# Kernel optimization log

Measured on AMD Instinct MI355X. Metric: run time of the kernel, lower is better.

The kernel has to match this reference:

```python
import jax, jax.numpy as jnp
import numpy as np

E, H, VS, VT, B, S, T = 256, 512, 32000, 32000, 64, 40, 40

def setup_inputs() -> dict:
    key = jax.random.key(0)
    ks = jax.random.split(key, 32)
    def n(k, shape, scale=0.05):
        return (jax.random.normal(k, shape, jnp.float32) * scale)
    return {
        "source_padded": jax.random.randint(ks[0], (B, S), 0, VS),
        "target_padded": jax.random.randint(ks[1], (B, T), 0, VT),
        "source_lengths": jax.random.randint(ks[2], (B,), 2, S + 1),
        "src_emb": n(ks[3], (VS, E)), "tgt_emb": n(ks[4], (VT, E)),
        "Wih_f": n(ks[5], (4 * H, E)), "Whh_f": n(ks[6], (4 * H, H)), "b_f": jnp.zeros((4 * H,), jnp.float32),
        "Wih_b": n(ks[7], (4 * H, E)), "Whh_b": n(ks[8], (4 * H, H)), "b_b": jnp.zeros((4 * H,), jnp.float32),
        "Wih_d": n(ks[9], (4 * H, H + E)), "Whh_d": n(ks[10], (4 * H, H)), "b_d": jnp.zeros((4 * H,), jnp.float32),
        "Whp": n(ks[11], (H, 2 * H)), "bhp": jnp.zeros((H,), jnp.float32),
        "Wcp": n(ks[12], (H, 2 * H)), "bcp": jnp.zeros((H,), jnp.float32),
        "Watt": n(ks[13], (H, 2 * H)), "batt": jnp.zeros((H,), jnp.float32),
        "Wcomb": n(ks[14], (H, 3 * H)), "bcomb": jnp.zeros((H,), jnp.float32),
        "Wvoc": n(ks[15], (VT, H)), "bvoc": jnp.zeros((VT,), jnp.float32),
    }

def _lstm_cell(x, h, c, Wih, Whh, b):
    g = x @ Wih.T + h @ Whh.T + b
    i, f, gg, o = jnp.split(g, 4, axis=-1)  # PyTorch gate order i,f,g,o
    c = jax.nn.sigmoid(f) * c + jax.nn.sigmoid(i) * jnp.tanh(gg)
    h = jax.nn.sigmoid(o) * jnp.tanh(c)
    return h, c

def _masked_scan(X, lengths, Wih, Whh, b):
    # X: [B,S,E]; emulates packed LSTM: state frozen and output zeroed past length
    Bn, Sn, _ = X.shape
    Hn = Whh.shape[1]
    def step(carry, inp):
        h, c = carry
        xt, t = inp
        hn, cn = _lstm_cell(xt, h, c, Wih, Whh, b)
        valid = (t < lengths)[:, None]
        h = jnp.where(valid, hn, h)
        c = jnp.where(valid, cn, c)
        return (h, c), jnp.where(valid, h, 0.0)
    init = (jnp.zeros((Bn, Hn), X.dtype), jnp.zeros((Bn, Hn), X.dtype))
    (h, c), outs = jax.lax.scan(step, init, (X.transpose(1, 0, 2), jnp.arange(Sn)))
    return outs.transpose(1, 0, 2), h, c

def _rev_in_len(X, lengths):
    # reverse each sequence within its own length, zeros elsewhere
    Sn = X.shape[1]
    idx = lengths[:, None] - 1 - jnp.arange(Sn)[None, :]
    g = jnp.take_along_axis(X, jnp.clip(idx, 0)[..., None], axis=1)
    return jnp.where((idx >= 0)[..., None], g, 0.0)

def _forward(source_padded, target_padded, source_lengths,
             src_emb, tgt_emb, Wih_f, Whh_f, b_f, Wih_b, Whh_b, b_b,
             Wih_d, Whh_d, b_d, Whp, bhp, Wcp, bcp, Watt, batt,
             Wcomb, bcomb, Wvoc, bvoc):
    X = src_emb[source_padded]                              # [B,S,E]
    out_f, hf, cf = _masked_scan(X, source_lengths, Wih_f, Whh_f, b_f)
    Xr = _rev_in_len(X, source_lengths)
    out_r, hb, cb = _masked_scan(Xr, source_lengths, Wih_b, Whh_b, b_b)
    out_b = _rev_in_len(out_r, source_lengths)
    enc_hidden = jnp.concatenate([out_f, out_b], axis=-1)   # [B,S,2H]
    dec_h = jnp.concatenate([hf, hb], axis=-1) @ Whp.T + bhp
    dec_c = jnp.concatenate([cf, cb], axis=-1) @ Wcp.T + bcp

    # generate_sent_masks: 1 at positions 1..len-1 (faithful to source), then masked_fill(-inf) where 1
    pos = jnp.arange(S)[None, :]
    enc_masks = (pos >= 1) & (pos < source_lengths[:, None])  # [B,S] bool

    enc_proj = enc_hidden @ Watt.T + batt                    # [B,S,H]
    Y = tgt_emb[target_padded]                               # [B,T,E]
    Hn = Whh_d.shape[1]
    o0 = jnp.zeros((B, Hn), jnp.float32)

    def dec_step(carry, y_t):
        h, c, o_prev = carry
        ybar = jnp.concatenate([y_t, o_prev], axis=-1)
        h, c = _lstm_cell(ybar, h, c, Wih_d, Whh_d, b_d)
        e = jnp.einsum('bsh,bh->bs', enc_proj, h)
        e = jnp.where(enc_masks, -jnp.inf, e)
        alpha = jax.nn.softmax(e, axis=-1)
        a = jnp.einsum('bs,bsd->bd', alpha, enc_hidden)      # [B,2H]
        U = jnp.concatenate([h, a], axis=-1)                 # [B,3H]
        O = jnp.tanh(U @ Wcomb.T + bcomb)                    # dropout eval-mode identity
        return (h, c, O), O

    _, outs = jax.lax.scan(dec_step, (dec_h, dec_c, o0), Y.transpose(1, 0, 2))  # [T,B,H]
    logits = outs @ Wvoc.T + bvoc                            # [T,B,VT]
    logp = jax.nn.log_softmax(logits, axis=-1)
    # CrossEntropyLoss(P.permute(1,2,0), target): mean NLL over all B*T positions
    tgt = target_padded.T[..., None]                         # [T,B,1]
    nll = -jnp.take_along_axis(logp, tgt, axis=-1).squeeze(-1)
    return nll.mean()

def reference(source_padded, target_padded, source_lengths,
              src_emb, tgt_emb, Wih_f, Whh_f, b_f, Wih_b, Whh_b, b_b,
              Wih_d, Whh_d, b_d, Whp, bhp, Wcp, bcp, Watt, batt,
              Wcomb, bcomb, Wvoc, bvoc):
    return _forward(source_padded, target_padded, source_lengths,
                    src_emb, tgt_emb, Wih_f, Whh_f, b_f, Wih_b, Whh_b, b_b,
                    Wih_d, Whh_d, b_d, Whp, bhp, Wcp, bcp, Watt, batt,
                    Wcomb, bcomb, Wvoc, bvoc)
```

## Files before the change

kernel.cpp:

```cpp
#include <hip/hip_runtime.h>
#include <math.h>

#define En 256
#define Hn 512
#define Bn 64
#define Sn 40
#define Tn 40
#define VTn 32000
#define Rn (Tn*Bn)
#define NCH 500

typedef short v8s __attribute__((ext_vector_type(8)));
typedef float v4f __attribute__((ext_vector_type(4)));
typedef _Float16 h2v __attribute__((ext_vector_type(2)));

#if defined(__has_builtin)
#  if __has_builtin(__builtin_amdgcn_fdot2)
#    define HAVE_FDOT2 1
#  endif
#endif

__device__ __forceinline__ float dot4(float4 a, float4 b){
  return a.x*b.x + a.y*b.y + a.z*b.z + a.w*b.w;
}
__device__ __forceinline__ float sigm(float x){ return 1.f/(1.f+__expf(-x)); }
__device__ __forceinline__ unsigned short f2bf(float f){
  unsigned u = __float_as_uint(f);
  unsigned r = u + 0x7FFFu + ((u>>16)&1u);
  return (unsigned short)(r>>16);
}
__device__ __forceinline__ float bf2f(unsigned short u){
  return __uint_as_float(((unsigned)u)<<16);
}
__device__ __forceinline__ unsigned pkbf(float a, float b){
  return (unsigned)f2bf(a) | ((unsigned)f2bf(b)<<16);
}
__device__ __forceinline__ unsigned pkh(float a, float b){
  _Float16 ha = (_Float16)a, hb = (_Float16)b;
  unsigned short ua = __builtin_bit_cast(unsigned short, ha);
  unsigned short ub = __builtin_bit_cast(unsigned short, hb);
  return (unsigned)ua | ((unsigned)ub<<16);
}
__device__ __forceinline__ float fd2(unsigned w, unsigned h, float c){
#ifdef HAVE_FDOT2
  return __builtin_amdgcn_fdot2(__builtin_bit_cast(h2v,w), __builtin_bit_cast(h2v,h), c, false);
#else
  h2v a = __builtin_bit_cast(h2v,w), b = __builtin_bit_cast(h2v,h);
  return c + (float)a[0]*(float)b[0] + (float)a[1]*(float)b[1];
#endif
}

__global__ void prep(float* zero_base,
                     const int* __restrict__ src, const int* __restrict__ tgt,
                     const int* __restrict__ lens, int* __restrict__ grev,
                     int* __restrict__ gtgt,
                     const float* __restrict__ Whh_f, unsigned short* __restrict__ Whf16,
                     const float* __restrict__ Whh_b, unsigned short* __restrict__ Whb16,
                     const float* __restrict__ Whh_d, const float* __restrict__ Wih_d,
                     unsigned short* __restrict__ Wd16,
                     const float* __restrict__ Wcomb, unsigned short* __restrict__ Wc16){
  int blk = blockIdx.x, tid = threadIdx.x;
  if (blk < 209){
    ((float4*)zero_base)[blk*256 + tid] = make_float4(0.f,0.f,0.f,0.f);
    return;
  }
  blk -= 209;
  if (blk < 10){
    int r = blk*256 + tid;
    if (r < Bn*Sn){
      int b = r/Sn, s = r%Sn;
      int j = lens[b]-1-s;
      grev[r] = (j>=0) ? src[b*Sn+j] : -1;
      int t2 = r>>6, b2 = r&63;
      gtgt[r] = tgt[b2*Tn + t2];
    }
    return;
  }
  blk -= 10;
  if (blk < 512){
    size_t e = ((size_t)blk*256 + tid)*8;
    float4 a = *(const float4*)(Whh_f+e), b = *(const float4*)(Whh_f+e+4);
    uint4 u; u.x=pkbf(a.x,a.y); u.y=pkbf(a.z,a.w); u.z=pkbf(b.x,b.y); u.w=pkbf(b.z,b.w);
    *(uint4*)(Whf16+e) = u;
    return;
  }
  blk -= 512;
  if (blk < 512){
    size_t e = ((size_t)blk*256 + tid)*8;
    float4 a = *(const float4*)(Whh_b+e), b = *(const float4*)(Whh_b+e+4);
    uint4 u; u.x=pkbf(a.x,a.y); u.y=pkbf(a.z,a.w); u.z=pkbf(b.x,b.y); u.w=pkbf(b.z,b.w);
    *(uint4*)(Whb16+e) = u;
    return;
  }
  blk -= 512;
  if (blk < 1024){
    size_t e = ((size_t)blk*256 + tid)*8;
    int row = (int)(e>>10), k = (int)(e&1023);
    const float* sp = (k<512) ? (Whh_d + (size_t)row*512 + k)
                              : (Wih_d + (size_t)row*768 + 256 + (k-512));
    float4 a = *(const float4*)sp, b = *(const float4*)(sp+4);
    uint4 u; u.x=pkbf(a.x,a.y); u.y=pkbf(a.z,a.w); u.z=pkbf(b.x,b.y); u.w=pkbf(b.z,b.w);
    *(uint4*)(Wd16+e) = u;
    return;
  }
  blk -= 1024;
  {
    size_t e = ((size_t)blk*256 + tid)*8;
    float4 a = *(const float4*)(Wcomb+e), b = *(const float4*)(Wcomb+e+4);
    uint4 u; u.x=pkh(a.x,a.y); u.y=pkh(a.z,a.w); u.z=pkh(b.x,b.y); u.w=pkh(b.z,b.w);
    *(uint4*)(Wc16+e) = u;
  }
}

struct GArg {
  const float* A; const int* gth; int lda;
  const float* B; int ldb;
  const float* bias; float* C; int ldc; int K;
};
struct GArg3 { GArg a[3]; };

__global__ __launch_bounds__(256) void ggemm(GArg3 p3){
  GArg d = p3.a[blockIdx.z];
  __shared__ unsigned short Abf[128*64];
  __shared__ unsigned short Bbf[128*64];
  const int n0 = blockIdx.x*128, r0 = blockIdx.y*128;
  const int tid = threadIdx.x;
  const int w = tid>>6, lane = tid&63;
  const int wr = w>>1, wc = w&1;
  v4f acc[4][4];
#pragma unroll
  for (int i=0;i<4;++i)
#pragma unroll
    for (int j=0;j<4;++j) acc[i][j] = (v4f){0.f,0.f,0.f,0.f};
  const int srow = tid>>1, kc = (tid&1)*32;
  int ar = d.gth ? d.gth[r0+srow] : (r0+srow);
  const float* Arow = (ar>=0) ? (d.A + (size_t)ar*d.lda) : nullptr;
  const float* Brow = d.B + (size_t)(n0+srow)*d.ldb;
  for (int kb=0; kb<d.K; kb+=64){
    __syncthreads();
#pragma unroll
    for (int c=0;c<4;++c){
      int k = kc + c*8;
      int swz = k ^ ((srow&7)<<3);
      uint4 ua;
      if (Arow){
        float4 x0 = *(const float4*)(Arow+kb+k);
        float4 x1 = *(const float4*)(Arow+kb+k+4);
        ua.x=pkbf(x0.x,x0.y); ua.y=pkbf(x0.z,x0.w); ua.z=pkbf(x1.x,x1.y); ua.w=pkbf(x1.z,x1.w);
      } else ua = make_uint4(0,0,0,0);
      *(uint4*)&Abf[srow*64 + swz] = ua;
      float4 y0 = *(const float4*)(Brow+kb+k);
      float4 y1 = *(const float4*)(Brow+kb+k+4);
      uint4 ub; ub.x=pkbf(y0.x,y0.y); ub.y=pkbf(y0.z,y0.w); ub.z=pkbf(y1.x,y1.y); ub.w=pkbf(y1.z,y1.w);
      *(uint4*)&Bbf[srow*64 + swz] = ub;
    }
    __syncthreads();
#pragma unroll
    for (int kk=0; kk<64; kk+=32){
      int kfr = kk + (lane>>4)*8;
      v8s bfr[4];
#pragma unroll
      for (int ni=0;ni<4;++ni){
        int brow = wc*64 + ni*16 + (lane&15);
        bfr[ni] = *(const v8s*)&Bbf[brow*64 + (kfr ^ ((brow&7)<<3))];
      }
#pragma unroll
      for (int mi=0;mi<4;++mi){
        int arl = wr*64 + mi*16 + (lane&15);
        v8s af = *(const v8s*)&Abf[arl*64 + (kfr ^ ((arl&7)<<3))];
#pragma unroll
        for (int ni=0;ni<4;++ni)
          acc[mi][ni] = __builtin_amdgcn_mfma_f32_16x16x32_bf16(af, bfr[ni], acc[mi][ni], 0,0,0);
      }
    }
  }
#pragma unroll
  for (int ni=0;ni<4;++ni){
    int col = n0 + wc*64 + ni*16 + (lane&15);
    float bb = d.bias[col];
#pragma unroll
    for (int mi=0;mi<4;++mi)
#pragma unroll
      for (int r=0;r<4;++r){
        int row = r0 + wr*64 + mi*16 + (lane>>4)*4 + r;
        d.C[(size_t)row*d.ldc + col] = acc[mi][ni][r] + bb;
      }
  }
}

__global__ __launch_bounds__(256) void enc_step(
    const unsigned short* __restrict__ hf_in, unsigned short* __restrict__ hf_out,
    const unsigned short* __restrict__ hb_in, unsigned short* __restrict__ hb_out,
    float* __restrict__ cF, float* __restrict__ cB,
    const unsigned short* __restrict__ Wf16, const unsigned short* __restrict__ Wb16,
    const float* __restrict__ Gf, const float* __restrict__ Gb,
    float* __restrict__ encH, float* __restrict__ outR,
    const int* __restrict__ lens,
    const float* __restrict__ Wvoc, unsigned short* __restrict__ W16, int s){
  const int bxall = blockIdx.x;
  const int tid = threadIdx.x;
  if (bxall >= 64){
    int chunk = s*200 + (bxall - 64);
    if (chunk < 8000){
      size_t e = ((size_t)chunk*256 + tid)*8;
      float4 a = *(const float4*)(Wvoc+e), b = *(const float4*)(Wvoc+e+4);
      uint4 u; u.x=pkbf(a.x,a.y); u.y=pkbf(a.z,a.w); u.z=pkbf(b.x,b.y); u.w=pkbf(b.z,b.w);
      *(uint4*)(W16+e) = u;
    }
    return;
  }
  __shared__ unsigned short Wls[64*64];
  __shared__ unsigned short Hls[64*64];
  __shared__ float Cls[64][66];
  const int bx = bxall;
  const int dir = bx>>5;
  const int u0 = (bx&31)*16;
  const unsigned short* Wm16 = dir ? Wb16 : Wf16;
  const unsigned short* hin = dir ? hb_in : hf_in;
  unsigned short* hout      = dir ? hb_out : hf_out;
  float* c = dir ? cB : cF;
  const float* G = dir ? Gb : Gf;
  const int w = tid>>6, lane = tid&63;
  v4f acc[4];
#pragma unroll
  for (int ni=0;ni<4;++ni) acc[ni] = (v4f){0.f,0.f,0.f,0.f};
  const int l = tid>>2;
  const int kc4 = (tid&3)*16;
  const int grow = (l>>4)*512 + u0 + (l&15);
  const unsigned short* Wrow = Wm16 + (size_t)grow*512;
  const unsigned short* Hrow = hin + (size_t)l*512;
  for (int kb=0; kb<512; kb+=64){
    __syncthreads();
#pragma unroll
    for (int c2=0;c2<2;++c2){
      int k = kc4 + c2*8;
      int swz = k ^ ((l&7)<<3);
      *(uint4*)&Wls[l*64+swz] = *(const uint4*)(Wrow + kb + k);
      *(uint4*)&Hls[l*64+swz] = *(const uint4*)(Hrow + kb + k);
    }
    __syncthreads();
#pragma unroll
    for (int kk=0; kk<64; kk+=32){
      int kfr = kk + (lane>>4)*8;
      int mrow = w*16 + (lane&15);
      v8s af = *(const v8s*)&Wls[mrow*64 + (kfr ^ ((mrow&7)<<3))];
#pragma unroll
      for (int ni=0;ni<4;++ni){
        int brow = ni*16 + (lane&15);
        v8s bf = *(const v8s*)&Hls[brow*64 + (kfr ^ ((brow&7)<<3))];
        acc[ni] = __builtin_amdgcn_mfma_f32_16x16x32_bf16(af, bf, acc[ni], 0,0,0);
      }
    }
  }
#pragma unroll
  for (int ni=0;ni<4;++ni)
#pragma unroll
    for (int r=0;r<4;++r)
      Cls[w*16 + (lane>>4)*4 + r][ni*16 + (lane&15)] = acc[ni][r];
  __syncthreads();
  const int u_l = tid&15, bq = tid>>4;
#pragma unroll
  for (int j=0;j<4;++j){
    int b = bq + j*16;
    size_t gidx = ((size_t)(b*Sn+s))*2048 + u0 + u_l;
    float gi = Cls[u_l][b]      + G[gidx];
    float gf = Cls[16+u_l][b]   + G[gidx+512];
    float gg = Cls[32+u_l][b]   + G[gidx+1024];
    float go = Cls[48+u_l][b]   + G[gidx+1536];
    int bu = b*512 + u0 + u_l;
    bool valid = s < lens[b];
    float cp = c[bu];
    float cn = sigm(gf)*cp + sigm(gi)*tanhf(gg);
    float hn = sigm(go)*tanhf(cn);
    c[bu] = valid ? cn : cp;
    hout[bu] = valid ? f2bf(hn) : hin[bu];
    if (dir==0) encH[((size_t)(b*Sn+s))*1024 + u0+u_l] = valid ? hn : 0.f;
    else        outR[((size_t)(b*Sn+s))*512  + u0+u_l] = valid ? hn : 0.f;
  }
}

__global__ void mid_fused(const unsigned short* __restrict__ h16f,
                          const unsigned short* __restrict__ h16b,
                          const float* __restrict__ cF, const float* __restrict__ cB,
                          const float* __restrict__ Whp, const float* __restrict__ bhp,
                          const float* __restrict__ Wcp, const float* __restrict__ bcp,
                          unsigned short* __restrict__ ho0, float* __restrict__ dC,
                          const float* __restrict__ outR, const int* __restrict__ lens,
                          float* __restrict__ encH){
  int blk = blockIdx.x, tid = threadIdx.x;
  if (blk < 128){
    int isC = blk >= 64;
    int idx = (blk & 63)*256 + tid;
#pragma unroll
    for (int e=0;e<2;++e){
      int o = idx*2 + e;
      int b = o>>9, u = o&511;
      if (!isC){
        const float* wr = Whp + (size_t)u*1024;
        float acc = bhp[u];
        const uint4* hf4 = (const uint4*)(h16f + (size_t)b*512);
        for (int q=0;q<64;++q){
          uint4 v = hf4[q];
          unsigned uu[4] = {v.x,v.y,v.z,v.w};
#pragma unroll
          for (int i2=0;i2<4;++i2){
            acc += bf2f((unsigned short)(uu[i2]&0xFFFF))*wr[q*8+i2*2];
            acc += bf2f((unsigned short)(uu[i2]>>16))   *wr[q*8+i2*2+1];
          }
        }
        const uint4* hb4 = (const uint4*)(h16b + (size_t)b*512);
        const float* wr2 = wr + 512;
        for (int q=0;q<64;++q){
          uint4 v = hb4[q];
          unsigned uu[4] = {v.x,v.y,v.z,v.w};
#pragma unroll
          for (int i2=0;i2<4;++i2){
            acc += bf2f((unsigned short)(uu[i2]&0xFFFF))*wr2[q*8+i2*2];
            acc += bf2f((unsigned short)(uu[i2]>>16))   *wr2[q*8+i2*2+1];
          }
        }
        ho0[b*1024 + u] = f2bf(acc);
      } else {
        const float4* w4 = (const float4*)(Wcp + (size_t)u*1024);
        float acc = bcp[u];
        const float4* x1 = (const float4*)(cF + (size_t)b*512);
        const float4* x2 = (const float4*)(cB + (size_t)b*512);
        for (int q=0;q<128;++q) acc += dot4(x1[q], w4[q]);
        for (int q=0;q<128;++q) acc += dot4(x2[q], w4[128+q]);
        dC[b*512 + u] = acc;
      }
    }
    return;
  }
  blk -= 128;
  {
    int e = (blk*256 + tid)*8;
    int u = e & 511;
    int bsi = e >> 9;
    int s = bsi % Sn, b = bsi / Sn;
    int len = lens[b];
    float4 v0 = make_float4(0,0,0,0), v1 = make_float4(0,0,0,0);
    if (s < len){
      int j = len-1-s;
      const float* sp = outR + ((size_t)(b*Sn+j))*512 + u;
      v0 = *(const float4*)sp; v1 = *(const float4*)(sp+4);
    }
    float* dp = encH + ((size_t)(b*Sn+s))*1024 + 512 + u;
    *(float4*)dp = v0; *(float4*)(dp+4) = v1;
  }
}

__global__ __launch_bounds__(256) void dec_gates(
    const unsigned short* __restrict__ Wd16, const unsigned short* __restrict__ ho_cur,
    unsigned short* __restrict__ ho_next, const float* __restrict__ Gdy,
    float* __restrict__ dC, int t){
  __shared__ unsigned short Wls[64*64];
  __shared__ unsigned short Hls[64*64];
  __shared__ float Cls[64][66];
  const int u0 = blockIdx.x*16;
  const int tid = threadIdx.x, w = tid>>6, lane = tid&63;
  v4f acc[4];
#pragma unroll
  for (int ni=0;ni<4;++ni) acc[ni] = (v4f){0.f,0.f,0.f,0.f};
  const int l = tid>>2;
  const int kc4 = (tid&3)*16;
  const int grow = (l>>4)*512 + u0 + (l&15);
  const unsigned short* Wrow = Wd16 + (size_t)grow*1024;
  const unsigned short* Hrow = ho_cur + (size_t)l*1024;
  for (int kb=0; kb<1024; kb+=64){
    __syncthreads();
#pragma unroll
    for (int c2=0;c2<2;++c2){
      int k = kc4 + c2*8;
      int swz = k ^ ((l&7)<<3);
      *(uint4*)&Wls[l*64+swz] = *(const uint4*)(Wrow + kb + k);
      *(uint4*)&Hls[l*64+swz] = *(const uint4*)(Hrow + kb + k);
    }
    __syncthreads();
#pragma unroll
    for (int kk=0; kk<64; kk+=32){
      int kfr = kk + (lane>>4)*8;
      int mrow = w*16 + (lane&15);
      v8s af = *(const v8s*)&Wls[mrow*64 + (kfr ^ ((mrow&7)<<3))];
#pragma unroll
      for (int ni=0;ni<4;++ni){
        int brow = ni*16 + (lane&15);
        v8s bf = *(const v8s*)&Hls[brow*64 + (kfr ^ ((brow&7)<<3))];
        acc[ni] = __builtin_amdgcn_mfma_f32_16x16x32_bf16(af, bf, acc[ni], 0,0,0);
      }
    }
  }
#pragma unroll
  for (int ni=0;ni<4;++ni)
#pragma unroll
    for (int r=0;r<4;++r)
      Cls[w*16 + (lane>>4)*4 + r][ni*16 + (lane&15)] = acc[ni][r];
  __syncthreads();
  const int u_l = tid&15, bq = tid>>4;
#pragma unroll
  for (int j=0;j<4;++j){
    int b = bq + j*16;
    size_t gidx = ((size_t)(t*Bn+b))*2048 + u0 + u_l;
    float gi = Cls[u_l][b]      + Gdy[gidx];
    float gf = Cls[16+u_l][b]   + Gdy[gidx+512];
    float gg = Cls[32+u_l][b]   + Gdy[gidx+1024];
    float go = Cls[48+u_l][b]   + Gdy[gidx+1536];
    int bu = b*512 + u0 + u_l;
    float cp = dC[bu];
    float cn = sigm(gf)*cp + sigm(gi)*tanhf(gg);
    float hn = sigm(go)*tanhf(cn);
    dC[bu] = cn;
    ho_next[b*1024 + u0 + u_l] = f2bf(hn);
  }
}

__global__ __launch_bounds__(256) void dec_attcomb(
    unsigned short* __restrict__ ho_next, const float* __restrict__ eprj,
    const float* __restrict__ encH, const int* __restrict__ lens,
    const unsigned short* __restrict__ Wc16, const float* __restrict__ bcomb,
    unsigned short* __restrict__ A16, int t){
  const int b = blockIdx.x >> 2;
  const int q = blockIdx.x & 3;
  const int tid = threadIdx.x;
  __shared__ __align__(16) float hs[512];
  __shared__ __align__(16) float als[1024];
  __shared__ float es[Sn], sal[Sn];
  __shared__ float sinv;
  __shared__ __align__(16) unsigned int ha16[768];
  __shared__ float ps[128][2];
  for (int i=tid; i<512; i+=256) hs[i] = bf2f(ho_next[b*1024 + i]);
  __syncthreads();
  const int wv = tid>>6, lane = tid&63;
  const int len = lens[b];
  for (int si=0; si<10; ++si){
    int s2 = wv*10 + si;
    const float* pr = eprj + ((size_t)(b*Sn+s2))*512 + lane*8;
    float4 p0 = *(const float4*)pr, p1 = *(const float4*)(pr+4);
    const float* hh = hs + lane*8;
    float4 h0 = *(const float4*)hh, h1 = *(const float4*)(hh+4);
    float a = dot4(p0,h0) + dot4(p1,h1);
#pragma unroll
    for (int off=32; off; off>>=1) a += __shfl_down(a, off);
    if (lane==0) es[s2] = (s2>=1 && s2<len) ? -INFINITY : a;
  }
  __syncthreads();
  if (tid < 64){
    float e2 = (tid<Sn) ? es[tid] : -INFINITY;
    float m = e2;
#pragma unroll
    for (int off=32; off; off>>=1) m = fmaxf(m, __shfl_xor(m, off));
    float p = (tid<Sn) ? __expf(e2-m) : 0.f;
    float sum = p;
#pragma unroll
    for (int off=32; off; off>>=1) sum += __shfl_xor(sum, off);
    if (tid<Sn) sal[tid] = p;
    if (tid==0) sinv = 1.f/sum;
  }
  __syncthreads();
  float inv = sinv;
#pragma unroll
  for (int dq=0; dq<4; ++dq){
    int d = dq*256 + tid;
    float acc = 0.f;
    for (int s2=0; s2<Sn; ++s2) acc += sal[s2]*encH[((size_t)(b*Sn+s2))*1024 + d];
    als[d] = acc*inv;
  }
  __syncthreads();
  for (int p=tid; p<768; p+=256){
    int i0 = 2*p, i1 = 2*p+1;
    float x0 = (i0<512) ? hs[i0] : als[i0-512];
    float x1 = (i1<512) ? hs[i1] : als[i1-512];
    ha16[p] = pkh(x0, x1);
  }
  __syncthreads();
  const int rloc = tid & 127;
  const int kh = tid >> 7;
  const int row = q*128 + rloc;
  const uint4* wp = (const uint4*)(Wc16 + (size_t)row*1536 + kh*768);
  const uint4* hp = (const uint4*)&ha16[kh*384];
  float a0 = 0.f;
#pragma unroll 4
  for (int qq=0; qq<96; ++qq){
    uint4 wv4 = wp[qq];
    uint4 hv4 = hp[qq];
    a0 = fd2(wv4.x, hv4.x, a0);
    a0 = fd2(wv4.y, hv4.y, a0);
    a0 = fd2(wv4.z, hv4.z, a0);
    a0 = fd2(wv4.w, hv4.w, a0);
  }
  ps[rloc][kh] = a0;
  __syncthreads();
  if (tid < 128){
    int r2 = q*128 + tid;
    float O = tanhf(ps[tid][0] + ps[tid][1] + bcomb[r2]);
    unsigned short ob = f2bf(O);
    ho_next[b*1024 + 512 + r2] = ob;
    A16[((size_t)(t*Bn+b))*512 + r2] = ob;
  }
}

__global__ __launch_bounds__(256) void vocab_mfma(
    const unsigned short* __restrict__ A16, const unsigned short* __restrict__ W16,
    const float* __restrict__ bv, float* __restrict__ stats){
  __shared__ unsigned short Abf[128*64];
  __shared__ unsigned short Bbf[128*64];
  const int vb = blockIdx.x, rb = blockIdx.y;
  const int r0 = rb*128, v0 = vb*128;
  const int tid = threadIdx.x;
  const int w = tid>>6, lane = tid&63;
  const int wr = w>>1, wc = w&1;
  v4f acc[4][4];
#pragma unroll
  for (int i=0;i<4;++i)
#pragma unroll
    for (int j=0;j<4;++j) acc[i][j] = (v4f){0.f,0.f,0.f,0.f};
  const int srow = tid>>1;
  const int sk0  = (tid&1)*8;
  const int arow = wr*64 + (lane&15);
  const int brow = wc*64 + (lane&15);
  const int kfrag = (lane>>4)*8;
  for (int ks=0; ks<8; ++ks){
    const int kb = ks*64;
    __syncthreads();
#pragma unroll
    for (int c=0;c<4;++c){
      int k = sk0 + c*16;
      int swz = k ^ ((srow&7)<<3);
      *(uint4*)&Abf[srow*64 + swz] = *(const uint4*)(A16 + (size_t)(r0+srow)*512 + kb + k);
      *(uint4*)&Bbf[srow*64 + swz] = *(const uint4*)(W16 + (size_t)(v0+srow)*512 + kb + k);
    }
    __syncthreads();
#pragma unroll
    for (int kk=0; kk<64; kk+=32){
      v8s af[4], bf[4];
#pragma unroll
      for (int mi=0;mi<4;++mi){
        int row = arow + mi*16;
        int k = kk + kfrag;
        af[mi] = *(const v8s*)&Abf[row*64 + (k ^ ((row&7)<<3))];
      }
#pragma unroll
      for (int ni=0;ni<4;++ni){
        int row = brow + ni*16;
        int k = kk + kfrag;
        bf[ni] = *(const v8s*)&Bbf[row*64 + (k ^ ((row&7)<<3))];
      }
#pragma unroll
      for (int mi=0;mi<4;++mi)
#pragma unroll
        for (int ni=0;ni<4;++ni)
          acc[mi][ni] = __builtin_amdgcn_mfma_f32_16x16x32_bf16(af[mi], bf[ni], acc[mi][ni], 0,0,0);
    }
  }
  float bj[4];
#pragma unroll
  for (int ni=0;ni<4;++ni) bj[ni] = bv[v0 + wc*64 + ni*16 + (lane&15)];
#pragma unroll
  for (int mi=0;mi<4;++mi){
#pragma unroll
    for (int r=0;r<4;++r){
      float x0 = acc[mi][0][r]+bj[0], x1 = acc[mi][1][r]+bj[1];
      float x2 = acc[mi][2][r]+bj[2], x3 = acc[mi][3][r]+bj[3];
      float mx = fmaxf(fmaxf(x0,x1), fmaxf(x2,x3));
#pragma unroll
      for (int off=1; off<16; off<<=1) mx = fmaxf(mx, __shfl_xor(mx, off));
      float se = __expf(x0-mx)+__expf(x1-mx)+__expf(x2-mx)+__expf(x3-mx);
#pragma unroll
      for (int off=1; off<16; off<<=1) se += __shfl_xor(se, off);
      if ((lane&15)==0){
        int row = r0 + wr*64 + mi*16 + (lane>>4)*4 + r;
        int chunk = vb*2 + wc;
        size_t o = ((size_t)row*NCH + chunk)*2;
        stats[o]   = mx;
        stats[o+1] = se;
      }
    }
  }
}

__global__ void tail(const float* __restrict__ stats, const unsigned short* __restrict__ A16,
                     const float* __restrict__ Wvoc, const float* __restrict__ bvoc,
                     const int* __restrict__ gtgt, float* __restrict__ out){
  int r = blockIdx.x*4 + (threadIdx.x>>6);
  int lane = threadIdx.x & 63;
  const float* st = stats + (size_t)r*NCH*2;
  float M = -INFINITY;
  for (int c=lane; c<NCH; c+=64) M = fmaxf(M, st[2*c]);
#pragma unroll
  for (int off=32; off; off>>=1) M = fmaxf(M, __shfl_xor(M, off));
  float S = 0.f;
  for (int c=lane; c<NCH; c+=64) S += __expf(st[2*c]-M)*st[2*c+1];
#pragma unroll
  for (int off=32; off; off>>=1) S += __shfl_xor(S, off);
  int v = gtgt[r];
  int k = lane*8;
  uint4 a4 = *(const uint4*)(A16 + (size_t)r*512 + k);
  const float* wvp = Wvoc + (size_t)v*512 + k;
  float4 w0 = *(const float4*)wvp, w1 = *(const float4*)(wvp+4);
  unsigned uu[4] = {a4.x, a4.y, a4.z, a4.w};
  float dot = 0.f;
  dot += bf2f((unsigned short)(uu[0]&0xFFFF))*w0.x + bf2f((unsigned short)(uu[0]>>16))*w0.y;
  dot += bf2f((unsigned short)(uu[1]&0xFFFF))*w0.z + bf2f((unsigned short)(uu[1]>>16))*w0.w;
  dot += bf2f((unsigned short)(uu[2]&0xFFFF))*w1.x + bf2f((unsigned short)(uu[2]>>16))*w1.y;
  dot += bf2f((unsigned short)(uu[3]&0xFFFF))*w1.z + bf2f((unsigned short)(uu[3]>>16))*w1.w;
#pragma unroll
  for (int off=32; off; off>>=1) dot += __shfl_down(dot, off);
  if (lane==0){
    float lse = M + logf(S);
    float nll = lse - (dot + bvoc[v]);
    atomicAdd(out, nll * (1.0f/(float)Rn));
  }
}

extern "C" void kernel_launch(void* const* d_in, const int* in_sizes, int n_in,
                              void* d_out, int out_size, void* d_ws, size_t ws_size,
                              hipStream_t stream){
  (void)in_sizes; (void)n_in; (void)out_size; (void)ws_size;
  const int*   srcP  = (const int*)  d_in[0];
  const int*   tgtP  = (const int*)  d_in[1];
  const int*   lens  = (const int*)  d_in[2];
  const float* semb  = (const float*)d_in[3];
  const float* temb  = (const float*)d_in[4];
  const float* Wih_f = (const float*)d_in[5];
  const float* Whh_f = (const float*)d_in[6];
  const float* b_f   = (const float*)d_in[7];
  const float* Wih_b = (const float*)d_in[8];
  const float* Whh_b = (const float*)d_in[9];
  const float* b_b   = (const float*)d_in[10];
  const float* Wih_d = (const float*)d_in[11];
  const float* Whh_d = (const float*)d_in[12];
  const float* b_d   = (const float*)d_in[13];
  const float* Whp   = (const float*)d_in[14];
  const float* bhp   = (const float*)d_in[15];
  const float* Wcp   = (const float*)d_in[16];
  const float* bcp   = (const float*)d_in[17];
  const float* Watt  = (const float*)d_in[18];
  const float* batt  = (const float*)d_in[19];
  const float* Wcomb = (const float*)d_in[20];
  const float* bcomb = (const float*)d_in[21];
  const float* Wvoc  = (const float*)d_in[22];
  const float* bvoc  = (const float*)d_in[23];

  float* w = (float*)d_ws;
  size_t off = 0;
  auto alloc = [&](size_t n){ float* p = w + off; off += n; return p; };
  float* encH = alloc(2621440);
  float* outR = alloc(1310720);
  float* eprj = alloc(1310720);
  float* Gf   = alloc(5242880);
  float* Gb   = alloc(5242880);
  float* Gdy  = alloc(5242880);
  unsigned short* W16   = (unsigned short*)alloc((size_t)VTn*Hn/2);
  unsigned short* A16   = (unsigned short*)alloc(655360);
  unsigned short* Whf16 = (unsigned short*)alloc(524288);
  unsigned short* Whb16 = (unsigned short*)alloc(524288);
  unsigned short* Wd16  = (unsigned short*)alloc(1048576);
  unsigned short* Wc16  = (unsigned short*)alloc(393216);
  float* zero_base = w + off;
  float* cF = alloc(32768);
  float* cB = alloc(32768);
  float* dC = alloc(32768);
  unsigned short* h16f0 = (unsigned short*)alloc(16384);
  unsigned short* h16f1 = (unsigned short*)alloc(16384);
  unsigned short* h16b0 = (unsigned short*)alloc(16384);
  unsigned short* h16b1 = (unsigned short*)alloc(16384);
  unsigned short* ho0   = (unsigned short*)alloc(32768);
  unsigned short* ho1   = (unsigned short*)alloc(32768);
  int* grev = (int*)alloc(2560);
  int* gtgt = (int*)alloc(2560);
  float* stats = encH;

  hipMemsetAsync(d_out, 0, sizeof(float), stream);
  prep<<<2651, 256, 0, stream>>>(zero_base, srcP, tgtP, lens, grev, gtgt,
                                 Whh_f, Whf16, Whh_b, Whb16, Whh_d, Wih_d, Wd16,
                                 Wcomb, Wc16);
  {
    GArg3 g;
    g.a[0] = GArg{semb, srcP, En, Wih_f, En,  b_f, Gf,  2048, En};
    g.a[1] = GArg{semb, grev, En, Wih_b, En,  b_b, Gb,  2048, En};
    g.a[2] = GArg{temb, gtgt, En, Wih_d, 768, b_d, Gdy, 2048, En};
    ggemm<<<dim3(16,20,3), 256, 0, stream>>>(g);
  }
  for (int s=0; s<Sn; ++s){
    const unsigned short* hfi = (s&1) ? h16f1 : h16f0;
    unsigned short*       hfo = (s&1) ? h16f0 : h16f1;
    const unsigned short* hbi = (s&1) ? h16b1 : h16b0;
    unsigned short*       hbo = (s&1) ? h16b0 : h16b1;
    enc_step<<<264, 256, 0, stream>>>(hfi, hfo, hbi, hbo, cF, cB,
                                      Whf16, Whb16, Gf, Gb, encH, outR, lens,
                                      Wvoc, W16, s);
  }
  mid_fused<<<768, 256, 0, stream>>>(h16f0, h16b0, cF, cB, Whp, bhp, Wcp, bcp,
                                     ho0, dC, outR, lens, encH);
  {
    GArg3 g;
    g.a[0] = GArg{encH, nullptr, 1024, Watt, 1024, batt, eprj, 512, 1024};
    g.a[1] = g.a[0]; g.a[2] = g.a[0];
    ggemm<<<dim3(4,20,1), 256, 0, stream>>>(g);
  }
  unsigned short* Hb[2] = {ho0, ho1};
  for (int t=0; t<Tn; ++t){
    dec_gates<<<32, 256, 0, stream>>>(Wd16, Hb[t&1], Hb[(t+1)&1], Gdy, dC, t);
    dec_attcomb<<<256, 256, 0, stream>>>(Hb[(t+1)&1], eprj, encH, lens, Wc16, bcomb, A16, t);
  }
  vocab_mfma<<<dim3(VTn/128, Rn/128), 256, 0, stream>>>(A16, W16, bvoc, stats);
  tail<<<Rn/4, 256, 0, stream>>>(stats, A16, Wvoc, bvoc, gtgt, (float*)d_out);
}
```

Measured before the change: 2.284 ms.

## Fuse 40 encoder step launches into one persistent batch-partitioned LSTM kernel

Replaces the per-timestep encoder launches with a single persistent kernel. Each of 16 blocks owns 8 batch rows for one direction and keeps h and c in shared memory across all 40 steps, so it only needs block-level barriers instead of kernel boundaries. The recurrent weights are repacked gate-interleaved so that each MFMA output tile yields the i, f, g and o gates for a unit directly. The trade-off is that each block streams the full 512x2048 weight matrix from L2 every step and only 16 blocks do the recurrence, with half of every MFMA tile's batch columns idle. The Wvoc conversion moves to a grid-stride loop over the remaining blocks.

```diff
diff --git a/kernel.cpp b/kernel.cpp
--- a/kernel.cpp
+++ b/kernel.cpp
@@ -79,17 +79,23 @@
   blk -= 10;
   if (blk < 512){
     size_t e = ((size_t)blk*256 + tid)*8;
-    float4 a = *(const float4*)(Whh_f+e), b = *(const float4*)(Whh_f+e+4);
-    uint4 u; u.x=pkbf(a.x,a.y); u.y=pkbf(a.z,a.w); u.z=pkbf(b.x,b.y); u.w=pkbf(b.z,b.w);
-    *(uint4*)(Whf16+e) = u;
+    int rowp = (int)(e>>9), k = (int)(e&511);
+    int u = rowp>>2, g = rowp&3;
+    const float* sp = Whh_f + ((size_t)(g*512+u))*512 + k;
+    float4 a = *(const float4*)sp, b = *(const float4*)(sp+4);
+    uint4 uo; uo.x=pkbf(a.x,a.y); uo.y=pkbf(a.z,a.w); uo.z=pkbf(b.x,b.y); uo.w=pkbf(b.z,b.w);
+    *(uint4*)(Whf16+e) = uo;
     return;
   }
   blk -= 512;
   if (blk < 512){
     size_t e = ((size_t)blk*256 + tid)*8;
-    float4 a = *(const float4*)(Whh_b+e), b = *(const float4*)(Whh_b+e+4);
-    uint4 u; u.x=pkbf(a.x,a.y); u.y=pkbf(a.z,a.w); u.z=pkbf(b.x,b.y); u.w=pkbf(b.z,b.w);
-    *(uint4*)(Whb16+e) = u;
+    int rowp = (int)(e>>9), k = (int)(e&511);
+    int u = rowp>>2, g = rowp&3;
+    const float* sp = Whh_b + ((size_t)(g*512+u))*512 + k;
+    float4 a = *(const float4*)sp, b = *(const float4*)(sp+4);
+    uint4 uo; uo.x=pkbf(a.x,a.y); uo.y=pkbf(a.z,a.w); uo.z=pkbf(b.x,b.y); uo.w=pkbf(b.z,b.w);
+    *(uint4*)(Whb16+e) = uo;
     return;
   }
   blk -= 512;
@@ -188,20 +194,17 @@
   }
 }
 
-__global__ __launch_bounds__(256) void enc_step(
-    const unsigned short* __restrict__ hf_in, unsigned short* __restrict__ hf_out,
-    const unsigned short* __restrict__ hb_in, unsigned short* __restrict__ hb_out,
-    float* __restrict__ cF, float* __restrict__ cB,
-    const unsigned short* __restrict__ Wf16, const unsigned short* __restrict__ Wb16,
+__global__ __launch_bounds__(256) void enc_all(
+    const unsigned short* __restrict__ Wpf, const unsigned short* __restrict__ Wpb,
     const float* __restrict__ Gf, const float* __restrict__ Gb,
     float* __restrict__ encH, float* __restrict__ outR,
+    unsigned short* __restrict__ hOutF, unsigned short* __restrict__ hOutB,
+    float* __restrict__ cOutF, float* __restrict__ cOutB,
     const int* __restrict__ lens,
-    const float* __restrict__ Wvoc, unsigned short* __restrict__ W16, int s){
-  const int bxall = blockIdx.x;
-  const int tid = threadIdx.x;
-  if (bxall >= 64){
-    int chunk = s*200 + (bxall - 64);
-    if (chunk < 8000){
+    const float* __restrict__ Wvoc, unsigned short* __restrict__ W16){
+  const int blk = blockIdx.x, tid = threadIdx.x;
+  if (blk >= 16){
+    for (int chunk = blk-16; chunk < 8000; chunk += 240){
       size_t e = ((size_t)chunk*256 + tid)*8;
       float4 a = *(const float4*)(Wvoc+e), b = *(const float4*)(Wvoc+e+4);
       uint4 u; u.x=pkbf(a.x,a.y); u.y=pkbf(a.z,a.w); u.z=pkbf(b.x,b.y); u.w=pkbf(b.z,b.w);
@@ -209,73 +212,70 @@
     }
     return;
   }
-  __shared__ unsigned short Wls[64*64];
-  __shared__ unsigned short Hls[64*64];
-  __shared__ float Cls[64][66];
-  const int bx = bxall;
-  const int dir = bx>>5;
-  const int u0 = (bx&31)*16;
-  const unsigned short* Wm16 = dir ? Wb16 : Wf16;
-  const unsigned short* hin = dir ? hb_in : hf_in;
-  unsigned short* hout      = dir ? hb_out : hf_out;
-  float* c = dir ? cB : cF;
+  const int dir = blk>>3, bg = blk&7;
+  const unsigned short* Wp = dir ? Wpb : Wpf;
   const float* G = dir ? Gb : Gf;
+  __shared__ unsigned short ho[2][16][520];
+  __shared__ float cs[8][512];
+  for (int i = tid; i < 2*16*520; i += 256) ((unsigned short*)ho)[i] = 0;
+  for (int i = tid; i < 8*512; i += 256) ((float*)cs)[i] = 0.f;
   const int w = tid>>6, lane = tid&63;
-  v4f acc[4];
-#pragma unroll
-  for (int ni=0;ni<4;++ni) acc[ni] = (v4f){0.f,0.f,0.f,0.f};
-  const int l = tid>>2;
-  const int kc4 = (tid&3)*16;
-  const int grow = (l>>4)*512 + u0 + (l&15);
-  const unsigned short* Wrow = Wm16 + (size_t)grow*512;
-  const unsigned short* Hrow = hin + (size_t)l*512;
-  for (int kb=0; kb<512; kb+=64){
+  const int lb = lane&15;
+  const int kq = lane>>4;
+  const bool active = lb < 8;
+  const int b = bg*8 + lb;
+  const int lenb = active ? lens[b] : 0;
+  __syncthreads();
+#pragma unroll 1
+  for (int s=0; s<Sn; ++s){
+    const int cur = s&1, nxt = cur^1;
+#pragma unroll 1
+    for (int mtg=0; mtg<8; ++mtg){
+      const int mt0 = w*32 + mtg*4;
+      v4f a0v={0.f,0.f,0.f,0.f}, a1v={0.f,0.f,0.f,0.f}, a2v={0.f,0.f,0.f,0.f}, a3v={0.f,0.f,0.f,0.f};
+      const unsigned short* wb = Wp + (size_t)(mt0*16 + lb)*512 + kq*8;
+#pragma unroll 4
+      for (int kk=0; kk<512; kk+=32){
+        v8s bf = *(const v8s*)&ho[cur][lb][kk + kq*8];
+        v8s wa0 = *(const v8s*)(wb + kk);
+        v8s wa1 = *(const v8s*)(wb + 16*512 + kk);
+        v8s wa2 = *(const v8s*)(wb + 32*512 + kk);
+        v8s wa3 = *(const v8s*)(wb + 48*512 + kk);
+        a0v = __builtin_amdgcn_mfma_f32_16x16x32_bf16(wa0, bf, a0v, 0,0,0);
+        a1v = __builtin_amdgcn_mfma_f32_16x16x32_bf16(wa1, bf, a1v, 0,0,0);
+        a2v = __builtin_amdgcn_mfma_f32_16x16x32_bf16(wa2, bf, a2v, 0,0,0);
+        a3v = __builtin_amdgcn_mfma_f32_16x16x32_bf16(wa3, bf, a3v, 0,0,0);
+      }
+      if (active){
+        const bool valid = s < lenb;
+        v4f av[4] = {a0v, a1v, a2v, a3v};
+#pragma unroll
+        for (int j=0;j<4;++j){
+          int u = (mt0+j)*4 + kq;
+          size_t gidx = ((size_t)(b*Sn+s))*2048 + u;
+          float gi = av[j][0] + G[gidx];
+          float gf = av[j][1] + G[gidx+512];
+          float gg = av[j][2] + G[gidx+1024];
+          float go = av[j][3] + G[gidx+1536];
+          float cp = cs[lb][u];
+          float cn = sigm(gf)*cp + sigm(gi)*tanhf(gg);
+          float hn = sigm(go)*tanhf(cn);
+          unsigned short hb_old = ho[cur][lb][u];
+          if (valid){ cs[lb][u] = cn; }
+          ho[nxt][lb][u] = valid ? f2bf(hn) : hb_old;
+          float outv = valid ? hn : 0.f;
+          if (dir==0) encH[((size_t)(b*Sn+s))*1024 + u] = outv;
+          else        outR[((size_t)(b*Sn+s))*512  + u] = outv;
+        }
+      }
+    }
     __syncthreads();
-#pragma unroll
-    for (int c2=0;c2<2;++c2){
-      int k = kc4 + c2*8;
-      int swz = k ^ ((l&7)<<3);
-      *(uint4*)&Wls[l*64+swz] = *(const uint4*)(Wrow + kb + k);
-      *(uint4*)&Hls[l*64+swz] = *(const uint4*)(Hrow + kb + k);
-    }
-    __syncthreads();
-#pragma unroll
-    for (int kk=0; kk<64; kk+=32){
-      int kfr = kk + (lane>>4)*8;
-      int mrow = w*16 + (lane&15);
-      v8s af = *(const v8s*)&Wls[mrow*64 + (kfr ^ ((mrow&7)<<3))];
-#pragma unroll
-      for (int ni=0;ni<4;++ni){
-        int brow = ni*16 + (lane&15);
-        v8s bf = *(const v8s*)&Hls[brow*64 + (kfr ^ ((brow&7)<<3))];
-        acc[ni] = __builtin_amdgcn_mfma_f32_16x16x32_bf16(af, bf, acc[ni], 0,0,0);
-      }
-    }
-  }
-#pragma unroll
-  for (int ni=0;ni<4;++ni)
-#pragma unroll
-    for (int r=0;r<4;++r)
-      Cls[w*16 + (lane>>4)*4 + r][ni*16 + (lane&15)] = acc[ni][r];
-  __syncthreads();
-  const int u_l = tid&15, bq = tid>>4;
-#pragma unroll
-  for (int j=0;j<4;++j){
-    int b = bq + j*16;
-    size_t gidx = ((size_t)(b*Sn+s))*2048 + u0 + u_l;
-    float gi = Cls[u_l][b]      + G[gidx];
-    float gf = Cls[16+u_l][b]   + G[gidx+512];
-    float gg = Cls[32+u_l][b]   + G[gidx+1024];
-    float go = Cls[48+u_l][b]   + G[gidx+1536];
-    int bu = b*512 + u0 + u_l;
-    bool valid = s < lens[b];
-    float cp = c[bu];
-    float cn = sigm(gf)*cp + sigm(gi)*tanhf(gg);
-    float hn = sigm(go)*tanhf(cn);
-    c[bu] = valid ? cn : cp;
-    hout[bu] = valid ? f2bf(hn) : hin[bu];
-    if (dir==0) encH[((size_t)(b*Sn+s))*1024 + u0+u_l] = valid ? hn : 0.f;
-    else        outR[((size_t)(b*Sn+s))*512  + u0+u_l] = valid ? hn : 0.f;
+  }
+  for (int i = tid; i < 8*512; i += 256){
+    int bl = i>>9, u = i&511;
+    int gb = bg*8 + bl;
+    if (dir==0){ hOutF[gb*512+u] = ho[0][bl][u]; cOutF[gb*512+u] = cs[bl][u]; }
+    else       { hOutB[gb*512+u] = ho[0][bl][u]; cOutB[gb*512+u] = cs[bl][u]; }
   }
 }
 
@@ -669,6 +669,7 @@
   int* grev = (int*)alloc(2560);
   int* gtgt = (int*)alloc(2560);
   float* stats = encH;
+  (void)h16f1; (void)h16b1;
 
   hipMemsetAsync(d_out, 0, sizeof(float), stream);
   prep<<<2651, 256, 0, stream>>>(zero_base, srcP, tgtP, lens, grev, gtgt,
@@ -681,15 +682,8 @@
     g.a[2] = GArg{temb, gtgt, En, Wih_d, 768, b_d, Gdy, 2048, En};
     ggemm<<<dim3(16,20,3), 256, 0, stream>>>(g);
   }
-  for (int s=0; s<Sn; ++s){
-    const unsigned short* hfi = (s&1) ? h16f1 : h16f0;
-    unsigned short*       hfo = (s&1) ? h16f0 : h16f1;
-    const unsigned short* hbi = (s&1) ? h16b1 : h16b0;
-    unsigned short*       hbo = (s&1) ? h16b0 : h16b1;
-    enc_step<<<264, 256, 0, stream>>>(hfi, hfo, hbi, hbo, cF, cB,
-                                      Whf16, Whb16, Gf, Gb, encH, outR, lens,
-                                      Wvoc, W16, s);
-  }
+  enc_all<<<256, 256, 0, stream>>>(Whf16, Whb16, Gf, Gb, encH, outR,
+                                   h16f0, h16b0, cF, cB, lens, Wvoc, W16);
   mid_fused<<<768, 256, 0, stream>>>(h16f0, h16b0, cF, cB, Whp, bhp, Wcp, bcp,
                                      ho0, dC, outR, lens, encH);
   {
```

New measurement: 4.762 ms. 2.08x slower.
